# Kernel optimization log

Hardware: AMD Instinct MI355X
Metric: run time of the kernel (lower is better)

Reference implementation:

```python
import jax, jax.numpy as jnp
import numpy as np

BER = 0.02          # ber_curve.ber_at(snr_db) evaluated at snr_db=10
BITS = 9            # ceil(log2(512)) for both coarse and fine codebooks
KC = 512
KF = 512
B, HC, WC, HF, WF, D = 64, 32, 32, 64, 64, 128


def _bitflip_channel(idx, u, bits, K):
    """Pack->bitflip->unpack->clip, vectorized.

    LSB-first packing of exactly bits-per-symbol means flipping bits of the
    packed byte stream == flipping each symbol's `bits` bits independently
    (flipped padding bits in the final byte are discarded by unpack).
    idx: [...] int32, u: [..., bits] float32 uniform(0,1).
    """
    shifts = jnp.arange(bits, dtype=jnp.int32)
    bitmat = (idx[..., None] >> shifts) & 1                       # [..., bits]
    flips = (u < BER).astype(jnp.int32)
    bitmat = jnp.bitwise_xor(bitmat, flips)
    rx = jnp.sum(bitmat << shifts, axis=-1)                       # [...]
    return jnp.clip(rx, 0, K - 1)


def setup_inputs() -> dict:
    key = jax.random.key(0)
    k1, k2, k3, k4, k5, k6 = jax.random.split(key, 6)
    return {
        "idx_c": jax.random.randint(k1, (B, HC, WC), 0, KC, dtype=jnp.int32),
        "idx_f": jax.random.randint(k2, (B, HF, WF), 0, KF, dtype=jnp.int32),
        "codebook_c": jax.random.normal(k3, (KC, D), dtype=jnp.float32),
        "codebook_f": jax.random.normal(k4, (KF, D), dtype=jnp.float32),
        "flip_u_c": jax.random.uniform(k5, (B, HC, WC, BITS), dtype=jnp.float32),
        "flip_u_f": jax.random.uniform(k6, (B, HF, WF, BITS), dtype=jnp.float32),
    }


def reference(idx_c, idx_f, codebook_c, codebook_f, flip_u_c, flip_u_f):
    rx_c = _bitflip_channel(idx_c, flip_u_c, BITS, KC)            # [B,Hc,Wc]
    rx_f = _bitflip_channel(idx_f, flip_u_f, BITS, KF)            # [B,Hf,Wf]
    # indices_to_quantized: embedding gather from each codebook
    q_coarse = codebook_c[rx_c]                                   # [B,Hc,Wc,D]
    q_fine = codebook_f[rx_f]                                     # [B,Hf,Wf,D]
    b = q_fine.shape[0]
    out = jnp.concatenate(
        [q_fine.reshape(b, -1), q_coarse.reshape(b, -1)], axis=1
    )
    return out
```

## Files before the change

kernel.cpp:

```cpp
#include <hip/hip_runtime.h>


constexpr int   BITS       = 9;
constexpr float BER        = 0.02f;
constexpr int   Bn         = 64;
constexpr int   HC = 32, WC = 32, HF = 64, WF = 64, D = 128;
constexpr int   NF         = Bn * HF * WF;
constexpr int   NC         = Bn * HC * WC;
constexpr int   NTOT       = NF + NC;
constexpr int   FINE_ROW   = HF * WF * D;
constexpr int   COARSE_ROW = HC * WC * D;
constexpr int   ROW        = FINE_ROW + COARSE_ROW;

__global__ __launch_bounds__(256) void flip_kernel(
    const int*   __restrict__ idx_c,
    const int*   __restrict__ idx_f,
    const float* __restrict__ u_c,
    const float* __restrict__ u_f,
    int*         __restrict__ rx)
{
    const int s = blockIdx.x * 256 + threadIdx.x;
    const float* u;  const int* idxp;  int local;
    if (s < NF) { u = u_f; idxp = idx_f; local = s; }
    else        { u = u_c; idxp = idx_c; local = s - NF; }
    const float* up = u + (size_t)local * BITS;
    int flip = 0;
    #pragma unroll
    for (int k = 0; k < BITS; ++k)
        flip |= (up[k] < BER) ? (1 << k) : 0;
    rx[s] = (idxp[local] ^ flip) & 511;
}

constexpr int GRID  = 2048;
constexpr int ITERS = NTOT / (8 * GRID);

__global__ __launch_bounds__(256) void gather_kernel(
    const float* __restrict__ cb_c,
    const float* __restrict__ cb_f,
    const int*   __restrict__ rx,
    float*       __restrict__ out)
{
    const int t          = threadIdx.x;
    const int sym_in_blk = t >> 5;
    const int lane32     = t & 31;

    #pragma unroll 2
    for (int it = 0; it < ITERS; ++it) {
        const int i = (it * GRID + blockIdx.x) * 8 + sym_in_blk;
        const int row = rx[i];

        const float* cb;  int off;
        if (i < NF) {
            const int b = i >> 12, rem = i & 4095;
            off = b * ROW + rem * D;                cb = cb_f;
        } else {
            const int j = i - NF;
            const int b = j >> 10, rem = j & 1023;
            off = b * ROW + FINE_ROW + rem * D;     cb = cb_c;
        }

        const float4 val = ((const float4*)(cb + row * D))[lane32];
        ((float4*)(out + off))[lane32] = val;
    }
}

extern "C" void kernel_launch(void* const* d_in, const int* in_sizes, int n_in,
                              void* d_out, int out_size, void* d_ws, size_t ws_size,
                              hipStream_t stream) {
    const int*   idx_c = (const int*)  d_in[0];
    const int*   idx_f = (const int*)  d_in[1];
    const float* cb_c  = (const float*)d_in[2];
    const float* cb_f  = (const float*)d_in[3];
    const float* u_c   = (const float*)d_in[4];
    const float* u_f   = (const float*)d_in[5];
    float*       out   = (float*)d_out;
    int*         rx    = (int*)d_ws;

    flip_kernel<<<NTOT / 256, 256, 0, stream>>>(idx_c, idx_f, u_c, u_f, rx);
    gather_kernel<<<GRID, 256, 0, stream>>>(cb_c, cb_f, rx, out);
}
```

Measured before the change: 185.4 us.

## Prefetch gather indices into LDS, split fine/coarse loops, use nontemporal stores

The gather kernel now loads all of a block's row indices into shared memory at the start and keeps them in registers. The single loop is split into separate fine and coarse loops, which removes the per-iteration branch, and both are fully unrolled. Output writes use nontemporal stores so the large write stream does not pollute the cache. The cost is extra register pressure from the unrolled loops and one block-level barrier.

```diff
diff --git a/kernel.cpp b/kernel.cpp
--- a/kernel.cpp
+++ b/kernel.cpp
@@ -1,5 +1,7 @@
 #include <hip/hip_runtime.h>
 
+
+typedef float f4 __attribute__((ext_vector_type(4)));
 
 constexpr int   BITS       = 9;
 constexpr float BER        = 0.02f;
@@ -31,8 +33,9 @@
     rx[s] = (idxp[local] ^ flip) & 511;
 }
 
-constexpr int GRID  = 2048;
-constexpr int ITERS = NTOT / (8 * GRID);
+constexpr int GRID       = 2048;
+constexpr int ITERS      = NTOT / (8 * GRID);
+constexpr int FINE_ITERS = NF   / (8 * GRID);
 
 __global__ __launch_bounds__(256) void gather_kernel(
     const float* __restrict__ cb_c,
@@ -40,27 +43,44 @@
     const int*   __restrict__ rx,
     float*       __restrict__ out)
 {
-    const int t          = threadIdx.x;
-    const int sym_in_blk = t >> 5;
-    const int lane32     = t & 31;
+    __shared__ int srow[ITERS * 8];
 
-    #pragma unroll 2
-    for (int it = 0; it < ITERS; ++it) {
-        const int i = (it * GRID + blockIdx.x) * 8 + sym_in_blk;
-        const int row = rx[i];
+    const int t = threadIdx.x;
 
-        const float* cb;  int off;
-        if (i < NF) {
-            const int b = i >> 12, rem = i & 4095;
-            off = b * ROW + rem * D;                cb = cb_f;
-        } else {
-            const int j = i - NF;
-            const int b = j >> 10, rem = j & 1023;
-            off = b * ROW + FINE_ROW + rem * D;     cb = cb_c;
-        }
+    if (t < ITERS * 8) {
+        const int chunk = (t >> 3) * GRID + blockIdx.x;
+        srow[t] = rx[chunk * 8 + (t & 7)];
+    }
+    __syncthreads();
 
-        const float4 val = ((const float4*)(cb + row * D))[lane32];
-        ((float4*)(out + off))[lane32] = val;
+    const int sym  = t >> 5;
+    const int lane = t & 31;
+
+    int row[ITERS];
+    #pragma unroll
+    for (int k = 0; k < ITERS; ++k)
+        row[k] = srow[k * 8 + sym];
+
+    const int base = blockIdx.x * 8 + sym;
+
+    #pragma unroll
+    for (int it = 0; it < FINE_ITERS; ++it) {
+        const int i   = it * (GRID * 8) + base;
+        const int b   = i >> 12;
+        const int rem = i & 4095;
+        const f4 v = ((const f4*)(cb_f + row[it] * D))[lane];
+        __builtin_nontemporal_store(
+            v, (f4*)(out + b * ROW + rem * D) + lane);
+    }
+
+    #pragma unroll
+    for (int it = FINE_ITERS; it < ITERS; ++it) {
+        const int j   = it * (GRID * 8) + base - NF;
+        const int b   = j >> 10;
+        const int rem = j & 1023;
+        const f4 v = ((const f4*)(cb_c + row[it] * D))[lane];
+        __builtin_nontemporal_store(
+            v, (f4*)(out + b * ROW + FINE_ROW + rem * D) + lane);
     }
 }
 
```

New measurement: 194.1 us. 4.7% more time.

## Fuse bitflip and gather kernels, staging received indices in shared memory

Applied to the files above, without the earlier changes.

Merges the flip kernel and the gather kernel into one launch. Each block decodes its own contiguous range of 160 symbols into LDS, then its waves copy the matching codebook rows to the output. This drops the rx workspace write and re-read, one kernel launch, and the inter-kernel dependency. The cost is that each block now waits on a serial flip phase before gathering, and only 160 of its 256 threads take part in that phase. The symbol-to-block mapping also changes from interleaved to contiguous, which alters the order in which output is written.

```diff
diff --git a/kernel.cpp b/kernel.cpp
--- a/kernel.cpp
+++ b/kernel.cpp
@@ -1,5 +1,7 @@
 #include <hip/hip_runtime.h>
 
+
+typedef float f4 __attribute__((ext_vector_type(4)));
 
 constexpr int   BITS       = 9;
 constexpr float BER        = 0.02f;
@@ -12,55 +14,61 @@
 constexpr int   COARSE_ROW = HC * WC * D;
 constexpr int   ROW        = FINE_ROW + COARSE_ROW;
 
-__global__ __launch_bounds__(256) void flip_kernel(
+constexpr int   GRID  = 2048;
+constexpr int   SPB   = NTOT / GRID;
+constexpr int   ITERS = SPB / 8;
+
+__global__ __launch_bounds__(256) void fused_kernel(
     const int*   __restrict__ idx_c,
     const int*   __restrict__ idx_f,
+    const float* __restrict__ cb_c,
+    const float* __restrict__ cb_f,
     const float* __restrict__ u_c,
     const float* __restrict__ u_f,
-    int*         __restrict__ rx)
-{
-    const int s = blockIdx.x * 256 + threadIdx.x;
-    const float* u;  const int* idxp;  int local;
-    if (s < NF) { u = u_f; idxp = idx_f; local = s; }
-    else        { u = u_c; idxp = idx_c; local = s - NF; }
-    const float* up = u + (size_t)local * BITS;
-    int flip = 0;
-    #pragma unroll
-    for (int k = 0; k < BITS; ++k)
-        flip |= (up[k] < BER) ? (1 << k) : 0;
-    rx[s] = (idxp[local] ^ flip) & 511;
-}
-
-constexpr int GRID  = 2048;
-constexpr int ITERS = NTOT / (8 * GRID);
-
-__global__ __launch_bounds__(256) void gather_kernel(
-    const float* __restrict__ cb_c,
-    const float* __restrict__ cb_f,
-    const int*   __restrict__ rx,
     float*       __restrict__ out)
 {
-    const int t          = threadIdx.x;
-    const int sym_in_blk = t >> 5;
-    const int lane32     = t & 31;
+    __shared__ int srow[SPB];
 
-    #pragma unroll 2
+    const int t  = threadIdx.x;
+    const int s0 = blockIdx.x * SPB;
+
+    if (t < SPB) {
+        const int i = s0 + t;
+        const float* up;  const int* idxp;  int local;
+        if (i < NF) { local = i;      up = u_f + (size_t)local * BITS; idxp = idx_f; }
+        else        { local = i - NF; up = u_c + (size_t)local * BITS; idxp = idx_c; }
+        int flip = 0;
+        #pragma unroll
+        for (int k = 0; k < BITS; ++k)
+            flip |= (up[k] < BER) ? (1 << k) : 0;
+        srow[t] = (idxp[local] ^ flip) & 511;
+    }
+    __syncthreads();
+
+    const int sym  = t >> 5;
+    const int lane = t & 31;
+
+    int row[ITERS];
+    #pragma unroll
+    for (int k = 0; k < ITERS; ++k)
+        row[k] = srow[k * 8 + sym];
+
+    #pragma unroll 4
     for (int it = 0; it < ITERS; ++it) {
-        const int i = (it * GRID + blockIdx.x) * 8 + sym_in_blk;
-        const int row = rx[i];
-
-        const float* cb;  int off;
+        const int i = s0 + it * 8 + sym;
+        const float* src;  int off;
         if (i < NF) {
             const int b = i >> 12, rem = i & 4095;
-            off = b * ROW + rem * D;                cb = cb_f;
+            src = cb_f + row[it] * D;
+            off = b * ROW + rem * D;
         } else {
             const int j = i - NF;
             const int b = j >> 10, rem = j & 1023;
-            off = b * ROW + FINE_ROW + rem * D;     cb = cb_c;
+            src = cb_c + row[it] * D;
+            off = b * ROW + FINE_ROW + rem * D;
         }
-
-        const float4 val = ((const float4*)(cb + row * D))[lane32];
-        ((float4*)(out + off))[lane32] = val;
+        const f4 v = ((const f4*)src)[lane];
+        ((f4*)(out + off))[lane] = v;
     }
 }
 
@@ -74,8 +82,7 @@
     const float* u_c   = (const float*)d_in[4];
     const float* u_f   = (const float*)d_in[5];
     float*       out   = (float*)d_out;
-    int*         rx    = (int*)d_ws;
+    (void)d_ws; (void)ws_size;
 
-    flip_kernel<<<NTOT / 256, 256, 0, stream>>>(idx_c, idx_f, u_c, u_f, rx);
-    gather_kernel<<<GRID, 256, 0, stream>>>(cb_c, cb_f, rx, out);
+    fused_kernel<<<GRID, 256, 0, stream>>>(idx_c, idx_f, cb_c, cb_f, u_c, u_f, out);
 }
```

Measured after the change: 183.7 us (median of 2 runs). No clear change (-0.9%).
